# Kernel tuning notes

Measured on AMD Instinct MI355X. Metric: run time of the kernel, lower is better.

The kernel has to match this reference:

```python
import jax, jax.numpy as jnp
import numpy as np

N, P, S = 512, 2048, 128  # diagrams, max points per diagram, phi samples


def setup_inputs() -> dict:
    key = jax.random.key(0)
    k1, k2, k3 = jax.random.split(key, 3)
    births = jax.random.uniform(k1, (N, P), dtype=jnp.float32)
    pers = jax.random.uniform(k2, (N, P), dtype=jnp.float32)
    diagrams = jnp.stack([births, births + pers], axis=-1)  # (N, P, 2) with death >= birth
    # ragged structure: each diagram has a variable number of valid points
    lens = jax.random.randint(k3, (N,), P // 4, P + 1)
    mask = jnp.arange(P)[None, :] < lens[:, None]  # bool (N, P)
    samples = jnp.linspace(0.0, 2.0, S, dtype=jnp.float32)
    theta = jnp.array([20.0], dtype=jnp.float32)
    constant = jnp.array([1.0], dtype=jnp.float32)
    power = jnp.array([1.0], dtype=jnp.float32)
    return {"diagrams": diagrams, "mask": mask, "samples": samples,
            "theta": theta, "constant": constant, "power": power}


def reference(diagrams, mask, samples, theta, constant, power):
    # phi = FlatPerslayPhi: sigmoid of a tent function evaluated at S sample points
    xs = diagrams[..., 0:1]  # (N, P, 1) births
    ys = diagrams[..., 1:2]  # (N, P, 1) deaths
    th = theta[0]
    # vector: (N, P, S)
    vector = jax.nn.sigmoid(th * (0.5 * (ys - xs)
                                  - jnp.abs(samples[None, None, :] - 0.5 * (ys + xs))))
    # weight = PowerPerslayWeight: constant * |death - birth| ** power, (N, P)
    w = constant[0] * jnp.power(jnp.abs(diagrams[..., 1] - diagrams[..., 0]), power[0])
    # ragged padding contributes 0 to the sum reduction
    w = jnp.where(mask, w, jnp.zeros_like(w))
    vector = vector * w[..., None]  # weight broadcast over phi output dims
    out = jnp.sum(vector, axis=1)   # perm_op = reduce_sum over points -> (N, S)
    return out                       # rho = identity
```

## Files before the change

kernel.cpp:

```cpp
#include <hip/hip_runtime.h>

#ifndef __has_builtin
#define __has_builtin(x) 0
#endif

#if __has_builtin(__builtin_amdgcn_exp2f)
#define FAST_EXP2(x) __builtin_amdgcn_exp2f(x)
#else
#define FAST_EXP2(x) __expf((x) * 0.69314718055994531f)
#endif
#if __has_builtin(__builtin_amdgcn_rcpf)
#define FAST_RCP(x) __builtin_amdgcn_rcpf(x)
#else
#define FAST_RCP(x) (1.0f / (x))
#endif

#define P_PTS 2048
#define S_SAMP 128
#define NTH 512

__global__ __launch_bounds__(NTH, 2) void perslay_kernel(
    const float* __restrict__ diagrams,
    const void*  __restrict__ maskp,
    const float* __restrict__ samples,
    const float* __restrict__ theta,
    const float* __restrict__ constant,
    const float* __restrict__ power,
    float* __restrict__ out)
{
    __shared__ float4 pts[P_PTS];
    __shared__ int    woff[33];
    __shared__ float  part[NTH];

    const int n    = blockIdx.x;
    const int tid  = threadIdx.x;
    const int lane = tid & 63;
    const int wid  = tid >> 6;

    const float th  = theta[0];
    const float cst = constant[0];
    const float pw  = power[0];
    const float c   = th * 1.4426950408889634f;
    const float a   = fabsf(c);
    const float sgn = (c >= 0.0f) ? 1.0f : -1.0f;

    const unsigned int* mw = (const unsigned int*)maskp;
    const bool isByte = (mw[0] > 1u) | (mw[1] > 1u) | (mw[2] > 1u) | (mw[3] > 1u);

    const float2* __restrict__ dg = ((const float2*)diagrams) + (size_t)n * P_PTS;

    float4 val[4];
    int    rank[4];
    bool   valid[4];

    #pragma unroll
    for (int r = 0; r < 4; ++r) {
        const int p = r * NTH + tid;
        const float2 xy = dg[p];
        bool m;
        if (isByte) m = ((const unsigned char*)maskp)[(size_t)n * P_PTS + p] != 0;
        else        m = ((const int*)maskp)[(size_t)n * P_PTS + p] != 0;
        const float pers = xy.y - xy.x;
        const float ap   = fabsf(pers);
        float w;
        if (pw == 1.0f)      w = cst * ap;
        else if (pw == 2.0f) w = cst * ap * ap;
        else                 w = cst * powf(ap, pw);
        valid[r] = m && (w != 0.0f);
        const float mid = 0.5f * (xy.x + xy.y);
        const float hf  = 0.5f * pers;
        val[r] = make_float4(a * mid, -c * hf, w, 0.0f);
        const unsigned long long b = __ballot(valid[r] ? 1 : 0);
        if (lane == 0) woff[r * 8 + wid] = (int)__popcll(b);
        rank[r] = (int)__popcll(b & ((1ull << lane) - 1ull));
    }
    __syncthreads();

    if (tid == 0) {
        int run = 0;
        #pragma unroll
        for (int j = 0; j < 32; ++j) { const int t = woff[j]; woff[j] = run; run += t; }
        woff[32] = run;
    }
    __syncthreads();

    #pragma unroll
    for (int r = 0; r < 4; ++r)
        if (valid[r]) pts[woff[r * 8 + wid] + rank[r]] = val[r];
    const int cnt = woff[32];
    __syncthreads();

    const int   q  = tid >> 7;
    const int   s  = tid & (S_SAMP - 1);
    const float sA = a * samples[s];

    float acc = 0.0f;
    const int i0 = (cnt * q) >> 2;
    const int i1 = (cnt * (q + 1)) >> 2;
    #pragma unroll 4
    for (int i = i0; i < i1; ++i) {
        const float4 v = pts[i];
        const float  d = sA - v.x;
        const float  u = fmaf(sgn, fabsf(d), v.y);
        const float  e = FAST_EXP2(u);
        acc = fmaf(v.z, FAST_RCP(1.0f + e), acc);
    }

    part[tid] = acc;
    __syncthreads();
    if (tid < S_SAMP) {
        const float rsum = part[tid] + part[tid + 128] + part[tid + 256] + part[tid + 384];
        out[(size_t)n * S_SAMP + tid] = rsum;
    }
}

extern "C" void kernel_launch(void* const* d_in, const int* in_sizes, int n_in,
                              void* d_out, int out_size, void* d_ws, size_t ws_size,
                              hipStream_t stream) {
    const float* diagrams = (const float*)d_in[0];
    const void*  mask     = d_in[1];
    const float* samples  = (const float*)d_in[2];
    const float* theta    = (const float*)d_in[3];
    const float* constant = (const float*)d_in[4];
    const float* power    = (const float*)d_in[5];
    float* out = (float*)d_out;

    const int N = in_sizes[0] / (2 * P_PTS);
    perslay_kernel<<<N, NTH, 0, stream>>>(diagrams, mask, samples, theta,
                                          constant, power, out);
}
```

Measured before the change: 101.1 us.

## Factor sigmoid exponent into per-point and per-sample exponentials, register-tile samples

Rewrites exp2(c*(hf - |s - mid|)) as a max/min of products of exponentials that are precomputed per point (exp(-c*y), exp(c*x)) and per sample (exp(±c*s)). This removes the transcendental from the inner loop, leaving two multiplies, a max/min, a reciprocal and an FMA. Each thread now holds 8 samples in registers against a strided group of points, and the result goes through a two-stage shared-memory reduction. The risks are overflow or underflow of the factored exponentials for large theta or coordinates, the extra shared-memory reduction, and the launch-bounds change to 4 blocks per SM, which adds register pressure.

```diff
diff --git a/kernel.cpp b/kernel.cpp
--- a/kernel.cpp
+++ b/kernel.cpp
@@ -7,7 +7,7 @@
 #if __has_builtin(__builtin_amdgcn_exp2f)
 #define FAST_EXP2(x) __builtin_amdgcn_exp2f(x)
 #else
-#define FAST_EXP2(x) __expf((x) * 0.69314718055994531f)
+#define FAST_EXP2(x) exp2f(x)
 #endif
 #if __has_builtin(__builtin_amdgcn_rcpf)
 #define FAST_RCP(x) __builtin_amdgcn_rcpf(x)
@@ -18,8 +18,10 @@
 #define P_PTS 2048
 #define S_SAMP 128
 #define NTH 512
+#define NG 32
+#define KS 8
 
-__global__ __launch_bounds__(NTH, 2) void perslay_kernel(
+__global__ __launch_bounds__(NTH, 4) void perslay_kernel(
     const float* __restrict__ diagrams,
     const void*  __restrict__ maskp,
     const float* __restrict__ samples,
@@ -30,7 +32,6 @@
 {
     __shared__ float4 pts[P_PTS];
     __shared__ int    woff[33];
-    __shared__ float  part[NTH];
 
     const int n    = blockIdx.x;
     const int tid  = threadIdx.x;
@@ -41,8 +42,6 @@
     const float cst = constant[0];
     const float pw  = power[0];
     const float c   = th * 1.4426950408889634f;
-    const float a   = fabsf(c);
-    const float sgn = (c >= 0.0f) ? 1.0f : -1.0f;
 
     const unsigned int* mw = (const unsigned int*)maskp;
     const bool isByte = (mw[0] > 1u) | (mw[1] > 1u) | (mw[2] > 1u) | (mw[3] > 1u);
@@ -67,9 +66,9 @@
         else if (pw == 2.0f) w = cst * ap * ap;
         else                 w = cst * powf(ap, pw);
         valid[r] = m && (w != 0.0f);
-        const float mid = 0.5f * (xy.x + xy.y);
-        const float hf  = 0.5f * pers;
-        val[r] = make_float4(a * mid, -c * hf, w, 0.0f);
+        const float A = FAST_EXP2(-c * xy.y);
+        const float B = FAST_EXP2( c * xy.x);
+        val[r] = make_float4(A, B, w, 0.0f);
         const unsigned long long b = __ballot(valid[r] ? 1 : 0);
         if (lane == 0) woff[r * 8 + wid] = (int)__popcll(b);
         rank[r] = (int)__popcll(b & ((1ull << lane) - 1ull));
@@ -87,30 +86,65 @@
     #pragma unroll
     for (int r = 0; r < 4; ++r)
         if (valid[r]) pts[woff[r * 8 + wid] + rank[r]] = val[r];
-    const int cnt = woff[32];
+    const int cnt    = woff[32];
+    const int padded = (cnt + NG - 1) & ~(NG - 1);
+    if (tid < padded - cnt) pts[cnt + tid] = make_float4(0.0f, 0.0f, 0.0f, 0.0f);
     __syncthreads();
 
-    const int   q  = tid >> 7;
-    const int   s  = tid & (S_SAMP - 1);
-    const float sA = a * samples[s];
+    const int   g     = tid >> 4;
+    const int   sbase = tid & 15;
 
-    float acc = 0.0f;
-    const int i0 = (cnt * q) >> 2;
-    const int i1 = (cnt * (q + 1)) >> 2;
-    #pragma unroll 4
-    for (int i = i0; i < i1; ++i) {
-        const float4 v = pts[i];
-        const float  d = sA - v.x;
-        const float  u = fmaf(sgn, fabsf(d), v.y);
-        const float  e = FAST_EXP2(u);
-        acc = fmaf(v.z, FAST_RCP(1.0f + e), acc);
+    float E[KS], rE[KS], acc[KS];
+    #pragma unroll
+    for (int k = 0; k < KS; ++k) {
+        const float sv = samples[sbase + 16 * k];
+        E[k]  = FAST_EXP2( c * sv);
+        rE[k] = FAST_EXP2(-c * sv);
+        acc[k] = 0.0f;
     }
 
-    part[tid] = acc;
+    const int jmax = padded >> 5;
+    const float4* __restrict__ pbase = pts + g;
+
+#define INNER_LOOP(SELFN)                                          \
+    _Pragma("unroll 2")                                            \
+    for (int j = 0; j < jmax; ++j) {                               \
+        const float4 v = pbase[j * NG];                            \
+        _Pragma("unroll")                                          \
+        for (int k = 0; k < KS; ++k) {                             \
+            const float t1 = E[k]  * v.x;                          \
+            const float t2 = rE[k] * v.y;                          \
+            const float u  = 1.0f + SELFN(t1, t2);                 \
+            acc[k] = fmaf(v.z, FAST_RCP(u), acc[k]);               \
+        }                                                          \
+    }
+
+    if (c >= 0.0f) { INNER_LOOP(fmaxf) } else { INNER_LOOP(fminf) }
+#undef INNER_LOOP
+
     __syncthreads();
+    float* part = (float*)pts;
+    #pragma unroll
+    for (int k = 0; k < KS; ++k)
+        part[g * S_SAMP + sbase + 16 * k] = acc[k];
+    __syncthreads();
+
+    float* part2 = part + NG * S_SAMP;
+    {
+        const int s  = tid & (S_SAMP - 1);
+        const int cq = tid >> 7;
+        float t = 0.0f;
+        #pragma unroll
+        for (int gg = 0; gg < 8; ++gg)
+            t += part[(cq * 8 + gg) * S_SAMP + s];
+        part2[cq * S_SAMP + s] = t;
+    }
+    __syncthreads();
+
     if (tid < S_SAMP) {
-        const float rsum = part[tid] + part[tid + 128] + part[tid + 256] + part[tid + 384];
-        out[(size_t)n * S_SAMP + tid] = rsum;
+        out[(size_t)n * S_SAMP + tid] =
+            (part2[tid] + part2[S_SAMP + tid]) +
+            (part2[2 * S_SAMP + tid] + part2[3 * S_SAMP + tid]);
     }
 }
 
```

New measurement: 92.07 us. 1.1x faster.

## Use persistent work-stealing blocks with factored exponentials and chunked point sweeps

Applied to the files above, without the earlier changes.

Replaces the per-diagram block with a persistent grid that claims 256-point chunks through an atomic counter, double-buffering chunk loads in shared memory and accumulating partial sums into the output with atomics. The sigmoid of the tent function is rewritten as a reciprocal of the max (or min) of two products built from precomputed per-sample and per-point exponentials, so the inner loop needs only FMAs, a max and a reciprocal and no per-pair exp2. Each thread now handles 8 samples across 16 point groups. In exchange it adds a memset and counter-init launch, global atomics, and possible overflow or underflow from exp2 of large arguments.

```diff
diff --git a/kernel.cpp b/kernel.cpp
--- a/kernel.cpp
+++ b/kernel.cpp
@@ -7,7 +7,7 @@
 #if __has_builtin(__builtin_amdgcn_exp2f)
 #define FAST_EXP2(x) __builtin_amdgcn_exp2f(x)
 #else
-#define FAST_EXP2(x) __expf((x) * 0.69314718055994531f)
+#define FAST_EXP2(x) exp2f(x)
 #endif
 #if __has_builtin(__builtin_amdgcn_rcpf)
 #define FAST_RCP(x) __builtin_amdgcn_rcpf(x)
@@ -15,24 +15,36 @@
 #define FAST_RCP(x) (1.0f / (x))
 #endif
 
-#define P_PTS 2048
+#define P_PTS  2048
 #define S_SAMP 128
-#define NTH 512
+#define ITEM   256
+#define IPD    (P_PTS / ITEM)
+#define NTH    256
+#define NG     16
+#define KS     8
+#define GRID   1536
 
-__global__ __launch_bounds__(NTH, 2) void perslay_kernel(
+
+__global__ void init_ctr_kernel(unsigned int* ctr, unsigned int v) {
+    if (threadIdx.x == 0 && blockIdx.x == 0) *ctr = v;
+}
+
+__global__ __launch_bounds__(NTH, 4) void perslay_kernel(
     const float* __restrict__ diagrams,
     const void*  __restrict__ maskp,
     const float* __restrict__ samples,
     const float* __restrict__ theta,
     const float* __restrict__ constant,
     const float* __restrict__ power,
-    float* __restrict__ out)
+    unsigned int* __restrict__ ctr,
+    float* __restrict__ out,
+    int nitems)
 {
-    __shared__ float4 pts[P_PTS];
-    __shared__ int    woff[33];
-    __shared__ float  part[NTH];
+    __shared__ float4 pts[2][ITEM + 2 * NG];
+    __shared__ float  part[2][NG * S_SAMP];
+    __shared__ int    woff[2][4];
+    __shared__ unsigned int nxt[2];
 
-    const int n    = blockIdx.x;
     const int tid  = threadIdx.x;
     const int lane = tid & 63;
     const int wid  = tid >> 6;
@@ -41,77 +53,115 @@
     const float cst = constant[0];
     const float pw  = power[0];
     const float c   = th * 1.4426950408889634f;
-    const float a   = fabsf(c);
-    const float sgn = (c >= 0.0f) ? 1.0f : -1.0f;
 
-    const unsigned int* mw = (const unsigned int*)maskp;
-    const bool isByte = (mw[0] > 1u) | (mw[1] > 1u) | (mw[2] > 1u) | (mw[3] > 1u);
+    const unsigned int* mwords = (const unsigned int*)maskp;
+    const bool isByte = (mwords[0] > 1u) | (mwords[1] > 1u) |
+                        (mwords[2] > 1u) | (mwords[3] > 1u);
 
-    const float2* __restrict__ dg = ((const float2*)diagrams) + (size_t)n * P_PTS;
-
-    float4 val[4];
-    int    rank[4];
-    bool   valid[4];
-
+    const int g = tid >> 4, sbase = tid & 15;
+    float E[KS], rE[KS], acc[KS];
     #pragma unroll
-    for (int r = 0; r < 4; ++r) {
-        const int p = r * NTH + tid;
-        const float2 xy = dg[p];
-        bool m;
-        if (isByte) m = ((const unsigned char*)maskp)[(size_t)n * P_PTS + p] != 0;
-        else        m = ((const int*)maskp)[(size_t)n * P_PTS + p] != 0;
-        const float pers = xy.y - xy.x;
-        const float ap   = fabsf(pers);
-        float w;
-        if (pw == 1.0f)      w = cst * ap;
-        else if (pw == 2.0f) w = cst * ap * ap;
-        else                 w = cst * powf(ap, pw);
-        valid[r] = m && (w != 0.0f);
-        const float mid = 0.5f * (xy.x + xy.y);
-        const float hf  = 0.5f * pers;
-        val[r] = make_float4(a * mid, -c * hf, w, 0.0f);
-        const unsigned long long b = __ballot(valid[r] ? 1 : 0);
-        if (lane == 0) woff[r * 8 + wid] = (int)__popcll(b);
-        rank[r] = (int)__popcll(b & ((1ull << lane) - 1ull));
-    }
-    __syncthreads();
-
-    if (tid == 0) {
-        int run = 0;
-        #pragma unroll
-        for (int j = 0; j < 32; ++j) { const int t = woff[j]; woff[j] = run; run += t; }
-        woff[32] = run;
-    }
-    __syncthreads();
-
-    #pragma unroll
-    for (int r = 0; r < 4; ++r)
-        if (valid[r]) pts[woff[r * 8 + wid] + rank[r]] = val[r];
-    const int cnt = woff[32];
-    __syncthreads();
-
-    const int   q  = tid >> 7;
-    const int   s  = tid & (S_SAMP - 1);
-    const float sA = a * samples[s];
-
-    float acc = 0.0f;
-    const int i0 = (cnt * q) >> 2;
-    const int i1 = (cnt * (q + 1)) >> 2;
-    #pragma unroll 4
-    for (int i = i0; i < i1; ++i) {
-        const float4 v = pts[i];
-        const float  d = sA - v.x;
-        const float  u = fmaf(sgn, fabsf(d), v.y);
-        const float  e = FAST_EXP2(u);
-        acc = fmaf(v.z, FAST_RCP(1.0f + e), acc);
+    for (int k = 0; k < KS; ++k) {
+        const float sv = samples[sbase + 16 * k];
+        E[k]  = FAST_EXP2( c * sv);
+        rE[k] = FAST_EXP2(-c * sv);
+        acc[k] = 0.0f;
     }
 
-    part[tid] = acc;
-    __syncthreads();
-    if (tid < S_SAMP) {
-        const float rsum = part[tid] + part[tid + 128] + part[tid + 256] + part[tid + 384];
-        out[(size_t)n * S_SAMP + tid] = rsum;
+    auto LOADI = [&](unsigned int idx, float2& xy, bool& m) {
+        xy = make_float2(0.0f, 0.0f); m = false;
+        if (idx < (unsigned)nitems) {
+            const size_t pb = (size_t)(idx / IPD) * P_PTS +
+                              (size_t)(idx % IPD) * ITEM + tid;
+            xy = ((const float2*)diagrams)[pb];
+            m  = isByte ? (((const unsigned char*)maskp)[pb] != 0)
+                        : (((const int*)maskp)[pb] != 0);
+        }
+    };
+    auto STORE = [&](int buf, float2 xy, bool m) {
+        float4 v = make_float4(0.0f, 0.0f, 0.0f, 0.0f);
+        if (m) {
+            const float pers = xy.y - xy.x;
+            const float ap   = fabsf(pers);
+            float w;
+            if (pw == 1.0f)      w = cst * ap;
+            else if (pw == 2.0f) w = cst * ap * ap;
+            else                 w = cst * powf(ap, pw);
+            v = make_float4(FAST_EXP2(-c * xy.y), FAST_EXP2(c * xy.x), w, 0.0f);
+        }
+        pts[buf][tid] = v;
+        const unsigned long long b = __ballot(m ? 1 : 0);
+        const int cand = b ? (wid * 64 + 64 - (int)__builtin_clzll(b)) : 0;
+        if (lane == 0) woff[buf][wid] = cand;
+    };
+
+#define EVAL(v, SELFN)                                             \
+    _Pragma("unroll")                                              \
+    for (int k = 0; k < KS; ++k) {                                 \
+        const float t1 = fmaf(E[k],  (v).x, 1.0f);                 \
+        const float t2 = fmaf(rE[k], (v).y, 1.0f);                 \
+        const float u  = SELFN(t1, t2);                            \
+        acc[k] = fmaf((v).z, FAST_RCP(u), acc[k]);                 \
     }
+
+#define SWEEP(BUF, CNT, SELFN)                                     \
+    {                                                              \
+        const int jmax = ((CNT + 31) >> 5) << 1;   \
+        const float4* __restrict__ pb = &pts[BUF][g];              \
+        if (jmax > 0) {                                            \
+            float4 b0 = pb[0], b1 = pb[NG];                        \
+            for (int j = 0; j < jmax; j += 2) {                    \
+                const float4 n0 = pb[(j + 2) * NG];  \
+                const float4 n1 = pb[(j + 3) * NG];                \
+                EVAL(b0, SELFN) EVAL(b1, SELFN)                    \
+                b0 = n0; b1 = n1;                                  \
+            }                                                      \
+        }                                                          \
+    }
+
+#define MAINLOOP(SELFN)                                                      \
+    {                                                                        \
+        unsigned int idx_cur = blockIdx.x;                                   \
+        float2 xy; bool m;                                                   \
+        LOADI(idx_cur, xy, m);                                               \
+        if (tid == 0) nxt[0] = atomicAdd(ctr, 1u);                           \
+        STORE(0, xy, m);                                                     \
+        __syncthreads();                                                     \
+        int cnt_cur = max(max(woff[0][0], woff[0][1]),                       \
+                          max(woff[0][2], woff[0][3]));                      \
+        unsigned int idx_next = nxt[0];                                      \
+        int p = 0;                                                           \
+        while (idx_cur < (unsigned)nitems) {                                 \
+            LOADI(idx_next, xy, m);                \
+            if (tid == 0) nxt[p ^ 1] = atomicAdd(ctr, 1u);                   \
+            SWEEP(p, cnt_cur, SELFN)                                         \
+            STORE(p ^ 1, xy, m);                                             \
+            _Pragma("unroll")                                                \
+            for (int k = 0; k < KS; ++k) {                                   \
+                part[p][g * S_SAMP + sbase + 16 * k] = acc[k];               \
+                acc[k] = 0.0f;                                               \
+            }                                                                \
+            __syncthreads();                                                 \
+            if (cnt_cur > 0 && tid < S_SAMP) {                               \
+                float t = 0.0f;                                              \
+                _Pragma("unroll")                                            \
+                for (int gg = 0; gg < NG; ++gg)                              \
+                    t += part[p][gg * S_SAMP + tid];                         \
+                atomicAdd(&out[(size_t)(idx_cur / IPD) * S_SAMP + tid], t);  \
+            }                                                                \
+            idx_cur  = idx_next;                                             \
+            cnt_cur  = max(max(woff[p ^ 1][0], woff[p ^ 1][1]),              \
+                           max(woff[p ^ 1][2], woff[p ^ 1][3]));             \
+            idx_next = nxt[p ^ 1];                                           \
+            p ^= 1;                                                          \
+        }                                                                    \
+    }
+
+    if (c >= 0.0f) MAINLOOP(fmaxf) else MAINLOOP(fminf)
+
+#undef MAINLOOP
+#undef SWEEP
+#undef EVAL
 }
 
 extern "C" void kernel_launch(void* const* d_in, const int* in_sizes, int n_in,
@@ -124,8 +174,13 @@
     const float* constant = (const float*)d_in[4];
     const float* power    = (const float*)d_in[5];
     float* out = (float*)d_out;
+    unsigned int* ctr = (unsigned int*)d_ws;
 
     const int N = in_sizes[0] / (2 * P_PTS);
-    perslay_kernel<<<N, NTH, 0, stream>>>(diagrams, mask, samples, theta,
-                                          constant, power, out);
+    const int nitems = N * IPD;
+
+    hipMemsetAsync(d_out, 0, (size_t)out_size * sizeof(float), stream);
+    init_ctr_kernel<<<1, 64, 0, stream>>>(ctr, (unsigned int)GRID);
+    perslay_kernel<<<GRID, NTH, 0, stream>>>(diagrams, mask, samples, theta,
+                                             constant, power, ctr, out, nitems);
 }
```

After: 140.7 us. 39.2% more time.
